# Performance work log

Measured on AMD Instinct MI355X. Metric: run time of the kernel, lower is better.

Reference implementation:

```python
import jax, jax.numpy as jnp
import numpy as np

B, L1, L2, H = 8, 384, 384, 128


def _lin(k, out_f, in_f, scale=0.05):
    kw, kb = jax.random.split(k)
    return (jax.random.normal(kw, (out_f, in_f), jnp.float32) * scale,
            jax.random.normal(kb, (out_f,), jnp.float32) * scale)


def setup_inputs() -> dict:
    key = jax.random.key(0)
    ks = jax.random.split(key, 10)
    Wq_w, Wq_b = _lin(ks[2], H, H)
    Wup_w, Wup_b = _lin(ks[3], H, H)
    Wvp_w, Wvp_b = _lin(ks[4], H, H)
    V_w, V_b = _lin(ks[5], 1, H)
    Wg_w, Wg_b = _lin(ks[6], 2 * H, 2 * H)
    W_ih, b_ih = _lin(ks[7], 4 * H, 2 * H)
    W_hh, b_hh = _lin(ks[8], 4 * H, H)
    return {
        "x": jax.random.normal(ks[0], (B, L1, H), jnp.float32),
        "x_mask": jnp.zeros((B, L1), dtype=bool),
        "y": jax.random.normal(ks[1], (B, L2, H), jnp.float32),
        "y_mask": jnp.zeros((B, L2), dtype=bool),
        "Wq_w": Wq_w, "Wq_b": Wq_b,
        "Wup_w": Wup_w, "Wup_b": Wup_b,
        "Wvp_w": Wvp_w, "Wvp_b": Wvp_b,
        "V_w": V_w, "V_b": V_b,
        "Wg_w": Wg_w, "Wg_b": Wg_b,
        "W_ih": W_ih, "W_hh": W_hh, "b_ih": b_ih, "b_hh": b_hh,
    }


def reference(x, x_mask, y, y_mask, Wq_w, Wq_b, Wup_w, Wup_b, Wvp_w, Wvp_b,
              V_w, V_b, Wg_w, Wg_b, W_ih, W_hh, b_ih, b_hh):
    b, l1, h = x.shape
    # projections (torch Linear: x @ W.T + b)
    x_proj = x @ Wup_w.T + Wup_b                      # [B, L1, H]
    y_proj = y @ Wq_w.T + Wq_b                        # [B, L2, H]
    # source feeds a constant zero hidden state into W_vp -> just its bias
    hidden_proj = jnp.zeros((h,), x.dtype) @ Wvp_w.T + Wvp_b  # [H]
    # additive attention scores: V . tanh(xp + yp + hp)
    sum_batch = jnp.tanh(x_proj[:, :, None, :] + y_proj[:, None, :, :] + hidden_proj)  # [B,L1,L2,H]
    s = jnp.einsum('btjh,h->btj', sum_batch, V_w[0]) + V_b[0]  # [B, L1, L2]
    # sum_mask = (1 - x_mask) outer (1 - y_mask)
    xm = 1.0 - x_mask.astype(s.dtype)
    ym = 1.0 - y_mask.astype(s.dtype)
    s = s * (xm[:, :, None] * ym[:, None, :])
    s = jnp.where(y_mask[:, None, :], -jnp.inf, s)
    alpha = jax.nn.softmax(s, axis=-1)                # [B, L1, L2]
    ct = jnp.einsum('btj,bjh->bth', alpha, y)         # [B, L1, H]
    merge = jnp.concatenate([x, ct], axis=2)          # [B, L1, 2H]
    gt = jax.nn.sigmoid(merge @ Wg_w.T + Wg_b)
    lstm_in = gt * merge                              # [B, L1, 2H]
    # single-layer unidirectional LSTM (torch gate order: i, f, g, o)
    gates_x = lstm_in @ W_ih.T + b_ih                 # [B, L1, 4H]

    def step(carry, gx):
        h_t, c_t = carry
        g = gx + h_t @ W_hh.T + b_hh
        i, f, gg, o = jnp.split(g, 4, axis=-1)
        c_n = jax.nn.sigmoid(f) * c_t + jax.nn.sigmoid(i) * jnp.tanh(gg)
        h_n = jax.nn.sigmoid(o) * jnp.tanh(c_n)
        return (h_n, c_n), h_n

    init = (jnp.zeros((b, h), x.dtype), jnp.zeros((b, h), x.dtype))
    _, hs = jax.lax.scan(step, init, jnp.swapaxes(gates_x, 0, 1))  # [L1, B, H]
    return jnp.swapaxes(hs, 0, 1)                     # [B, L1, H]
```

## Files before the change

### kernel.cpp

```cpp
#include <hip/hip_runtime.h>
#include <hip/hip_bf16.h>
#include <math.h>

typedef __attribute__((ext_vector_type(4))) float  float4v;
typedef __attribute__((ext_vector_type(2))) float  float2v;
typedef __attribute__((ext_vector_type(8))) short  short8;

#define B_ 8
#define L_ 384
#define H_ 128

__device__ __forceinline__ float bflo(unsigned int u){ unsigned int t = u << 16; float f; __builtin_memcpy(&f,&t,4); return f; }
__device__ __forceinline__ unsigned short f2bf(float f){
  unsigned int t; __builtin_memcpy(&t,&f,4);
  return (unsigned short)((t + 0x7fffu + ((t>>16)&1u)) >> 16);
}
__device__ __forceinline__ float fsig(float x){ return __fdividef(1.f, 1.f + __expf(-x)); }

__device__ __forceinline__ void barrier_lds(){
  asm volatile("s_waitcnt lgkmcnt(0)\n\ts_barrier" ::: "memory");
}

template<int K>
__device__ __forceinline__ void mfma_rowgemm_body(
    unsigned short* in_s,
    const float* __restrict__ inA,
    const float* __restrict__ W, const float* __restrict__ bias,
    const float* __restrict__ bias2, float* __restrict__ out,
    int Ntotal, int act, int row0, int ob)
{
  constexpr int KP = K + 2;
  const int tid  = threadIdx.x;
  const int w    = tid >> 6;
  const int l    = tid & 63;
  const int c    = l & 15;
  const int quad = l >> 4;

  #pragma unroll
  for (int it = 0; it < K/32; ++it) {
    int idx = it*256 + tid;
    int r = idx / (K/4);
    int k = (idx % (K/4)) * 4;
    float4v f = *(const float4v*)(inA + (size_t)(row0+r)*K + k);
    unsigned int p0 = (unsigned int)f2bf(f.x) | ((unsigned int)f2bf(f.y) << 16);
    unsigned int p1 = (unsigned int)f2bf(f.z) | ((unsigned int)f2bf(f.w) << 16);
    *(unsigned int*)&in_s[r*KP + k]     = p0;
    *(unsigned int*)&in_s[r*KP + k + 2] = p1;
  }

  const int n = ob + w*16 + c;
  short8 bfr[K/32];
  #pragma unroll
  for (int kt = 0; kt < K/32; ++kt) {
    const float* src = W + (size_t)n*K + kt*32 + quad*8;
    float4v f0 = *(const float4v*)(src);
    float4v f1 = *(const float4v*)(src + 4);
    short8 v;
    v[0]=(short)f2bf(f0[0]); v[1]=(short)f2bf(f0[1]); v[2]=(short)f2bf(f0[2]); v[3]=(short)f2bf(f0[3]);
    v[4]=(short)f2bf(f1[0]); v[5]=(short)f2bf(f1[1]); v[6]=(short)f2bf(f1[2]); v[7]=(short)f2bf(f1[3]);
    bfr[kt] = v;
  }
  __syncthreads();

  const float4v z4 = {0.f,0.f,0.f,0.f};
  float4v acc0 = z4, acc1 = z4;
  #pragma unroll
  for (int kt = 0; kt < K/32; ++kt) {
    short8 a0 = *(const short8*)&in_s[(c     )*KP + kt*32 + quad*8];
    short8 a1 = *(const short8*)&in_s[(16 + c)*KP + kt*32 + quad*8];
    acc0 = __builtin_amdgcn_mfma_f32_16x16x32_bf16(a0, bfr[kt], acc0, 0,0,0);
    acc1 = __builtin_amdgcn_mfma_f32_16x16x32_bf16(a1, bfr[kt], acc1, 0,0,0);
  }

  const float C2 = 2.8853900817779268f;
  float bv = bias[n] + (bias2 ? bias2[n] : 0.f);
  #pragma unroll
  for (int mt = 0; mt < 2; ++mt) {
    float4v A = mt ? acc1 : acc0;
    #pragma unroll
    for (int r = 0; r < 4; ++r) {
      int m = mt*16 + quad*4 + r;
      float val = A[r] + bv;
      if (act == 4)
        val = __builtin_amdgcn_exp2f(C2 * val);
      if (act == 3)
        out[(size_t)(row0+m)*Ntotal + (n & 127)*4 + (n >> 7)] = val;
      else
        out[(size_t)(row0+m)*Ntotal + n] = val;
    }
  }
}

template<int K>
__global__ __launch_bounds__(256) void mfma_rowgemm_kernel(
    const float* __restrict__ inA,
    const float* __restrict__ W, const float* __restrict__ bias,
    const float* __restrict__ bias2, float* __restrict__ out,
    int Ntotal, int act)
{
  __shared__ __align__(16) unsigned short in_s[32*(K+2)];
  mfma_rowgemm_body<K>(in_s, inA, W, bias, bias2, out,
                       Ntotal, act, blockIdx.x*32, blockIdx.y*64);
}

__global__ __launch_bounds__(256) void proj_mfma_kernel(
    const float* __restrict__ x, const float* __restrict__ y,
    const float* __restrict__ Wup_w, const float* __restrict__ Wup_b,
    const float* __restrict__ Wq_w, const float* __restrict__ Wq_b,
    const float* __restrict__ Wvp_b,
    float* __restrict__ xp, float* __restrict__ yp)
{
  __shared__ __align__(16) unsigned short in_s[32*130];
  int bx = blockIdx.x;
  if (bx < 192)
    mfma_rowgemm_body<128>(in_s, x, Wup_w, Wup_b, nullptr,
                           xp, 128, 4, (bx>>1)*32, (bx&1)*64);
  else {
    bx -= 192;
    mfma_rowgemm_body<128>(in_s, y, Wq_w, Wq_b, Wvp_b,
                           yp, 128, 4, (bx>>1)*32, (bx&1)*64);
  }
}

__global__ __launch_bounds__(256) void attn_kernel(
    const float* __restrict__ xp, const float* __restrict__ yp,
    const float* __restrict__ y, const unsigned char* __restrict__ xmask,
    const unsigned char* __restrict__ ymask, const float* __restrict__ Vw,
    const float* __restrict__ Vb,
    float* __restrict__ ctpbase, float* __restrict__ ml)
{
  __shared__ __align__(16) float xp_s[8][128];
  __shared__ __align__(16) float v2_s[128];
  __shared__ __align__(16) float yp_s[32][132];
  __shared__ __align__(16) float yc_s[32][132];
  __shared__ float xm_s[8];
  __shared__ float ym_s[32];
  __shared__ float sv_s;
  const int tid = threadIdx.x;
  const int b   = blockIdx.y;
  const int t0  = blockIdx.x * 8;
  const int jh  = blockIdx.z;
  const int jb  = jh * 96;
  {
    int r = tid >> 5, k4 = (tid & 31) * 4;
    float4v f = *(const float4v*)(xp + ((size_t)(b*L_ + t0 + r))*H_ + k4);
    *(float4v*)&xp_s[r][k4] = f;
    if (tid < 32) {
      float4v v = *(const float4v*)(Vw + tid*4);
      float4v v2; v2[0]=2.f*v[0]; v2[1]=2.f*v[1]; v2[2]=2.f*v[2]; v2[3]=2.f*v[3];
      *(float4v*)&v2_s[tid*4] = v2;
    }
    if (tid < 8) xm_s[tid] = xmask[b*L_ + t0 + tid] ? 0.f : 1.f;
  }
  __syncthreads();
  if (tid < 32) {
    float4v v = *(const float4v*)&v2_s[tid*4];
    float sm = (v[0]+v[1]) + (v[2]+v[3]);
    #pragma unroll
    for (int off = 16; off >= 1; off >>= 1) sm += __shfl_xor(sm, off);
    if (tid == 0) sv_s = 0.5f*sm + Vb[0];
  }

  float4v rp[4], ry[4];
  unsigned char ymb = 0;
  {
    #pragma unroll
    for (int it = 0; it < 4; ++it) {
      int idx = it*256 + tid; int r = idx >> 5; int k4 = (idx & 31) * 4;
      size_t base = ((size_t)(b*L_ + jb + r))*H_ + k4;
      rp[it] = *(const float4v*)(yp + base);
      ry[it] = *(const float4v*)(y + base);
    }
    if (tid < 32) ymb = ymask[b*L_ + jb + tid];
  }

  const int t = tid >> 5, u = tid & 31;
  float mrun = -__builtin_inff(), lrun = 0.f;
  float a0=0.f, a1=0.f, a2=0.f, a3=0.f;
  float svc = 0.f, xmv = 0.f;

  for (int c = 0; c < 3; ++c) {
    __syncthreads();
    #pragma unroll
    for (int it = 0; it < 4; ++it) {
      int idx = it*256 + tid; int r = idx >> 5; int k4 = (idx & 31) * 4;
      *(float4v*)&yp_s[r][k4] = rp[it];
      *(float4v*)&yc_s[r][k4] = ry[it];
    }
    if (tid < 32) ym_s[tid] = ymb ? 0.f : 1.f;
    __syncthreads();
    if (c == 0) { svc = sv_s; xmv = xm_s[t]; }
    if (c < 2) {
      #pragma unroll
      for (int it = 0; it < 4; ++it) {
        int idx = it*256 + tid; int r = idx >> 5; int k4 = (idx & 31) * 4;
        size_t base = ((size_t)(b*L_ + jb + (c+1)*32 + r))*H_ + k4;
        rp[it] = *(const float4v*)(yp + base);
        ry[it] = *(const float4v*)(y + base);
      }
      if (tid < 32) ymb = ymask[b*L_ + jb + (c+1)*32 + tid];
    }

    float sA = 0.f, sB = 0.f;
    {
      const float* yr = yp_s[u];
      const float* xr = xp_s[t];
      #pragma unroll 4
      for (int k = 0; k < 128; k += 4) {
        float4v yv = *(const float4v*)&yr[k];
        float4v xv = *(const float4v*)&xr[k];
        float4v vv = *(const float4v*)&v2_s[k];
        sA -= vv[0] * __builtin_amdgcn_rcpf(__builtin_fmaf(xv[0], yv[0], 1.f));
        sB -= vv[1] * __builtin_amdgcn_rcpf(__builtin_fmaf(xv[1], yv[1], 1.f));
        sA -= vv[2] * __builtin_amdgcn_rcpf(__builtin_fmaf(xv[2], yv[2], 1.f));
        sB -= vv[3] * __builtin_amdgcn_rcpf(__builtin_fmaf(xv[3], yv[3], 1.f));
      }
    }
    float ymv = ym_s[u];
    float s = (svc + sA + sB) * xmv * ymv;
    if (ymv == 0.f) s = -__builtin_inff();
    float mc = s;
    #pragma unroll
    for (int off = 16; off >= 1; off >>= 1) mc = fmaxf(mc, __shfl_xor(mc, off));
    float mnew = fmaxf(mrun, mc);
    float p  = __expf(s - mnew);
    float sc = __expf(mrun - mnew);
    float ps = p;
    #pragma unroll
    for (int off = 16; off >= 1; off >>= 1) ps += __shfl_xor(ps, off);
    lrun = lrun * sc + ps;
    mrun = mnew;
    a0 *= sc; a1 *= sc; a2 *= sc; a3 *= sc;
    #pragma unroll 8
    for (int j = 0; j < 32; ++j) {
      float pv = __shfl(p, j, 32);
      float4v yv = *(const float4v*)&yc_s[j][u*4];
      a0 += pv*yv[0]; a1 += pv*yv[1]; a2 += pv*yv[2]; a3 += pv*yv[3];
    }
  }
  const int row = b*L_ + t0 + t;
  float* ctp = ctpbase + (size_t)jh*393216;
  float4v ov; ov[0]=a0; ov[1]=a1; ov[2]=a2; ov[3]=a3;
  *(float4v*)(ctp + (size_t)row*H_ + u*4) = ov;
  if (u == 0) {
    ml[(jh*2+0)*3072 + row] = mrun;
    ml[(jh*2+1)*3072 + row] = lrun;
  }
}

__global__ __launch_bounds__(256) void gate1_kernel(
    const float* __restrict__ x,
    const float* __restrict__ ctpbase, const float* __restrict__ ml,
    const float* __restrict__ Wg_w, const float* __restrict__ Wg_b,
    float* __restrict__ out)
{
  constexpr int K = 256, KP = 258;
  __shared__ __align__(16) unsigned short in_s[32*KP];
  const int tid  = threadIdx.x;
  const int w    = tid >> 6;
  const int l    = tid & 63;
  const int c    = l & 15;
  const int quad = l >> 4;
  const int row0 = blockIdx.x * 32;
  const int ob   = blockIdx.y * 64;

  #pragma unroll
  for (int it = 0; it < 8; ++it) {
    int idx = it*256 + tid;
    int r = idx >> 6;
    int k = (idx & 63) * 4;
    int row = row0 + r;
    float4v f;
    if (k < 128) {
      f = *(const float4v*)(x + (size_t)row*128 + k);
    } else {
      float m0 = ml[       row], l0 = ml[  3072 + row];
      float m1 = ml[2*3072+row], l1 = ml[3*3072 + row];
      float m2 = ml[4*3072+row], l2 = ml[5*3072 + row];
      float m3 = ml[6*3072+row], l3 = ml[7*3072 + row];
      float mm = fmaxf(fmaxf(m0, m1), fmaxf(m2, m3));
      float e0 = __expf(m0-mm), e1 = __expf(m1-mm);
      float e2 = __expf(m2-mm), e3 = __expf(m3-mm);
      float inv = __fdividef(1.f, (l0*e0 + l1*e1) + (l2*e2 + l3*e3));
      size_t off = (size_t)row*128 + (k-128);
      float4v v0 = *(const float4v*)(ctpbase             + off);
      float4v v1 = *(const float4v*)(ctpbase +   393216  + off);
      float4v v2 = *(const float4v*)(ctpbase + 2*393216  + off);
      float4v v3 = *(const float4v*)(ctpbase + 3*393216  + off);
      f[0] = ((v0[0]*e0 + v1[0]*e1) + (v2[0]*e2 + v3[0]*e3))*inv;
      f[1] = ((v0[1]*e0 + v1[1]*e1) + (v2[1]*e2 + v3[1]*e3))*inv;
      f[2] = ((v0[2]*e0 + v1[2]*e1) + (v2[2]*e2 + v3[2]*e3))*inv;
      f[3] = ((v0[3]*e0 + v1[3]*e1) + (v2[3]*e2 + v3[3]*e3))*inv;
    }
    unsigned int p0 = (unsigned int)f2bf(f[0]) | ((unsigned int)f2bf(f[1]) << 16);
    unsigned int p1 = (unsigned int)f2bf(f[2]) | ((unsigned int)f2bf(f[3]) << 16);
    *(unsigned int*)&in_s[r*KP + k]     = p0;
    *(unsigned int*)&in_s[r*KP + k + 2] = p1;
  }

  const int n = ob + w*16 + c;
  short8 bfr[8];
  #pragma unroll
  for (int kt = 0; kt < 8; ++kt) {
    const float* src = Wg_w + (size_t)n*K + kt*32 + quad*8;
    float4v f0 = *(const float4v*)(src);
    float4v f1 = *(const float4v*)(src + 4);
    short8 v;
    v[0]=(short)f2bf(f0[0]); v[1]=(short)f2bf(f0[1]); v[2]=(short)f2bf(f0[2]); v[3]=(short)f2bf(f0[3]);
    v[4]=(short)f2bf(f1[0]); v[5]=(short)f2bf(f1[1]); v[6]=(short)f2bf(f1[2]); v[7]=(short)f2bf(f1[3]);
    bfr[kt] = v;
  }
  __syncthreads();

  const float4v z4 = {0.f,0.f,0.f,0.f};
  float4v acc0 = z4, acc1 = z4;
  #pragma unroll
  for (int kt = 0; kt < 8; ++kt) {
    short8 a0 = *(const short8*)&in_s[(c     )*KP + kt*32 + quad*8];
    short8 a1 = *(const short8*)&in_s[(16 + c)*KP + kt*32 + quad*8];
    acc0 = __builtin_amdgcn_mfma_f32_16x16x32_bf16(a0, bfr[kt], acc0, 0,0,0);
    acc1 = __builtin_amdgcn_mfma_f32_16x16x32_bf16(a1, bfr[kt], acc1, 0,0,0);
  }

  float bv = Wg_b[n];
  #pragma unroll
  for (int mt = 0; mt < 2; ++mt) {
    float4v A = mt ? acc1 : acc0;
    #pragma unroll
    for (int r = 0; r < 4; ++r) {
      int m = mt*16 + quad*4 + r;
      float val = A[r] + bv;
      float mg = bflo((unsigned int)in_s[m*KP + n]);
      out[(size_t)(row0+m)*256 + n] = fsig(val) * mg;
    }
  }
}

__global__ __launch_bounds__(512) void lstm_kernel(
    const float* __restrict__ gx, const float* __restrict__ Whh,
    float* __restrict__ out)
{
  __shared__ __align__(16) unsigned short h_s[2][128];
  const int tid  = threadIdx.x;
  const int b    = blockIdx.x;
  const int w    = tid >> 6;
  const int l    = tid & 63;
  const int col  = l & 15;
  const int quad = l >> 4;

  short8 bf[4][4];
  #pragma unroll
  for (int nt = 0; nt < 4; ++nt) {
    const int n = nt*128 + w*16 + col;
    #pragma unroll
    for (int kt = 0; kt < 4; ++kt) {
      const int k0 = kt*32 + quad*8;
      const float* src = Whh + (size_t)n*H_ + k0;
      float4v f0 = *(const float4v*)(src);
      float4v f1 = *(const float4v*)(src + 4);
      short8 v;
      v[0]=(short)f2bf(f0[0]); v[1]=(short)f2bf(f0[1]); v[2]=(short)f2bf(f0[2]); v[3]=(short)f2bf(f0[3]);
      v[4]=(short)f2bf(f1[0]); v[5]=(short)f2bf(f1[1]); v[6]=(short)f2bf(f1[2]); v[7]=(short)f2bf(f1[3]);
      bf[nt][kt] = v;
    }
  }

  if (tid < 128) { h_s[0][tid] = 0; h_s[1][tid] = 0; }
  float cst = 0.f;
  const int goff = w*16 + col;
  const float* gbase = gx + (size_t)b*L_*512 + goff*4;
  float* outp = out + (size_t)b*L_*H_ + goff;
  float4v gbuf[4];
  #pragma unroll
  for (int s = 0; s < 4; ++s)
    gbuf[s] = *(const float4v*)(gbase + (size_t)s*512);
  const float4v z4 = {0.f,0.f,0.f,0.f};
  const float NL2E = -1.4426950408889634f;
  const float P2L2E = 2.8853900817779268f;
  __syncthreads();

  for (int t4 = 0; t4 < L_; t4 += 4) {
    #pragma unroll
    for (int s = 0; s < 4; ++s) {
      const int tstep = t4 + s;
      const unsigned short* hb = h_s[s & 1];
      short8 a[4];
      #pragma unroll
      for (int kt=0;kt<4;++kt) a[kt] = *(const short8*)&hb[kt*32 + quad*8];
      float4v c0 = z4, c1 = z4, c2 = z4, c3 = z4;
      #pragma unroll
      for (int kt=0;kt<4;++kt) {
        c0 = __builtin_amdgcn_mfma_f32_16x16x32_bf16(a[kt], bf[0][kt], c0, 0,0,0);
        c1 = __builtin_amdgcn_mfma_f32_16x16x32_bf16(a[kt], bf[1][kt], c1, 0,0,0);
        c2 = __builtin_amdgcn_mfma_f32_16x16x32_bf16(a[kt], bf[2][kt], c2, 0,0,0);
        c3 = __builtin_amdgcn_mfma_f32_16x16x32_bf16(a[kt], bf[3][kt], c3, 0,0,0);
      }
      float g0 = c0[0] + gbuf[s][0];
      float g1 = c1[0] + gbuf[s][1];
      float g2 = c2[0] + gbuf[s][2];
      float g3 = c3[0] + gbuf[s][3];
      if (tstep + 4 < L_)
        gbuf[s] = *(const float4v*)(gbase + (size_t)(tstep+4)*512);
      if (quad == 0) {
        float ig = __builtin_amdgcn_rcpf(1.f + __builtin_amdgcn_exp2f(NL2E*g0));
        float fg = __builtin_amdgcn_rcpf(1.f + __builtin_amdgcn_exp2f(NL2E*g1));
        float gg = 1.f - 2.f*__builtin_amdgcn_rcpf(__builtin_amdgcn_exp2f(P2L2E*g2) + 1.f);
        float og = __builtin_amdgcn_rcpf(1.f + __builtin_amdgcn_exp2f(NL2E*g3));
        cst = fg*cst + ig*gg;
        float hn = og * (1.f - 2.f*__builtin_amdgcn_rcpf(__builtin_amdgcn_exp2f(P2L2E*cst) + 1.f));
        outp[(size_t)tstep*H_] = hn;
        h_s[(s+1)&1][goff] = f2bf(hn);
      }
      barrier_lds();
    }
  }
}

extern "C" void kernel_launch(void* const* d_in, const int* in_sizes, int n_in,
                              void* d_out, int out_size, void* d_ws, size_t ws_size,
                              hipStream_t stream)
{
  (void)in_sizes; (void)n_in; (void)out_size; (void)ws_size;
  const float* x     = (const float*)d_in[0];
  const unsigned char* xm = (const unsigned char*)d_in[1];
  const float* y     = (const float*)d_in[2];
  const unsigned char* ym = (const unsigned char*)d_in[3];
  const float* Wq_w  = (const float*)d_in[4];
  const float* Wq_b  = (const float*)d_in[5];
  const float* Wup_w = (const float*)d_in[6];
  const float* Wup_b = (const float*)d_in[7];
  const float* Wvp_b = (const float*)d_in[9];
  const float* V_w   = (const float*)d_in[10];
  const float* V_b   = (const float*)d_in[11];
  const float* Wg_w  = (const float*)d_in[12];
  const float* Wg_b  = (const float*)d_in[13];
  const float* W_ih  = (const float*)d_in[14];
  const float* W_hh  = (const float*)d_in[15];
  const float* b_ih  = (const float*)d_in[16];
  const float* b_hh  = (const float*)d_in[17];
  float* out = (float*)d_out;

  float* wsf    = (float*)d_ws;
  float* xp_ws  = wsf;
  float* yp_ws  = xp_ws + 393216;
  float* li_ws  = xp_ws;
  float* ctp_ws = yp_ws + 393216;
  float* gx_ws  = ctp_ws + 4*393216;
  float* ml_ws  = gx_ws + 1572864;

  proj_mfma_kernel<<<dim3(384),256,0,stream>>>(x, y, Wup_w, Wup_b, Wq_w, Wq_b, Wvp_b, xp_ws, yp_ws);
  attn_kernel<<<dim3(48,8,4),256,0,stream>>>(xp_ws, yp_ws, y, xm, ym, V_w, V_b, ctp_ws, ml_ws);
  gate1_kernel<<<dim3(96,4),256,0,stream>>>(x, ctp_ws, ml_ws, Wg_w, Wg_b, li_ws);
  mfma_rowgemm_kernel<256><<<dim3(96,8),256,0,stream>>>(li_ws, W_ih, b_ih, b_hh, gx_ws, 512, 3);
  lstm_kernel<<<dim3(8),512,0,stream>>>(gx_ws, W_hh, out);
}
```

Baseline: 336.6 us.

## Compute attention-weighted context with bf16 MFMA instead of scalar FMA loop

Replaces the per-thread scalar accumulation of alpha·y with 16x16x32 bf16 MFMA instructions. Probabilities are written to shared memory as bf16, padded to 16 rows, and y is loaded straight from global into register fragments converted to bf16, which removes the yc_s shared tile. This adds an extra barrier per chunk, uses half of the MFMA rows as padding, and lowers the precision of the context product to bf16.

```diff
diff --git a/kernel.cpp b/kernel.cpp
--- a/kernel.cpp
+++ b/kernel.cpp
@@ -132,7 +132,8 @@
   __shared__ __align__(16) float xp_s[8][128];
   __shared__ __align__(16) float v2_s[128];
   __shared__ __align__(16) float yp_s[32][132];
-  __shared__ __align__(16) float yc_s[32][132];
+  __shared__ __align__(16) unsigned short p_s[16][40];
+  __shared__ float sc_s[16];
   __shared__ float xm_s[8];
   __shared__ float ym_s[32];
   __shared__ float sv_s;
@@ -141,6 +142,10 @@
   const int t0  = blockIdx.x * 8;
   const int jh  = blockIdx.z;
   const int jb  = jh * 96;
+  const int w    = tid >> 6;
+  const int l    = tid & 63;
+  const int c16  = l & 15;
+  const int quad = l >> 4;
   {
     int r = tid >> 5, k4 = (tid & 31) * 4;
     float4v f = *(const float4v*)(xp + ((size_t)(b*L_ + t0 + r))*H_ + k4);
@@ -151,6 +156,8 @@
       *(float4v*)&v2_s[tid*4] = v2;
     }
     if (tid < 8) xm_s[tid] = xmask[b*L_ + t0 + tid] ? 0.f : 1.f;
+    if (tid < 16) sc_s[tid] = 0.f;
+    for (int i = 320 + tid; i < 640; i += 256) ((unsigned short*)p_s)[i] = 0;
   }
   __syncthreads();
   if (tid < 32) {
@@ -161,22 +168,21 @@
     if (tid == 0) sv_s = 0.5f*sm + Vb[0];
   }
 
-  float4v rp[4], ry[4];
+  float4v rp[4];
   unsigned char ymb = 0;
   {
     #pragma unroll
     for (int it = 0; it < 4; ++it) {
       int idx = it*256 + tid; int r = idx >> 5; int k4 = (idx & 31) * 4;
-      size_t base = ((size_t)(b*L_ + jb + r))*H_ + k4;
-      rp[it] = *(const float4v*)(yp + base);
-      ry[it] = *(const float4v*)(y + base);
+      rp[it] = *(const float4v*)(yp + ((size_t)(b*L_ + jb + r))*H_ + k4);
     }
     if (tid < 32) ymb = ymask[b*L_ + jb + tid];
   }
 
   const int t = tid >> 5, u = tid & 31;
   float mrun = -__builtin_inff(), lrun = 0.f;
-  float a0=0.f, a1=0.f, a2=0.f, a3=0.f;
+  const float4v z4 = {0.f,0.f,0.f,0.f};
+  float4v acc0 = z4, acc1 = z4;
   float svc = 0.f, xmv = 0.f;
 
   for (int c = 0; c < 3; ++c) {
@@ -185,18 +191,24 @@
     for (int it = 0; it < 4; ++it) {
       int idx = it*256 + tid; int r = idx >> 5; int k4 = (idx & 31) * 4;
       *(float4v*)&yp_s[r][k4] = rp[it];
-      *(float4v*)&yc_s[r][k4] = ry[it];
     }
     if (tid < 32) ym_s[tid] = ymb ? 0.f : 1.f;
     __syncthreads();
     if (c == 0) { svc = sv_s; xmv = xm_s[t]; }
+    short8 yb0, yb1;
+    {
+      const float* ybase = y + ((size_t)(b*L_ + jb + c*32 + quad*8))*H_ + c16;
+      #pragma unroll
+      for (int jj = 0; jj < 8; ++jj) {
+        yb0[jj] = (short)f2bf(ybase[(size_t)jj*H_ + w*16]);
+        yb1[jj] = (short)f2bf(ybase[(size_t)jj*H_ + (w+4)*16]);
+      }
+    }
     if (c < 2) {
       #pragma unroll
       for (int it = 0; it < 4; ++it) {
         int idx = it*256 + tid; int r = idx >> 5; int k4 = (idx & 31) * 4;
-        size_t base = ((size_t)(b*L_ + jb + (c+1)*32 + r))*H_ + k4;
-        rp[it] = *(const float4v*)(yp + base);
-        ry[it] = *(const float4v*)(y + base);
+        rp[it] = *(const float4v*)(yp + ((size_t)(b*L_ + jb + (c+1)*32 + r))*H_ + k4);
       }
       if (tid < 32) ymb = ymask[b*L_ + jb + (c+1)*32 + tid];
     }
@@ -230,19 +242,28 @@
     for (int off = 16; off >= 1; off >>= 1) ps += __shfl_xor(ps, off);
     lrun = lrun * sc + ps;
     mrun = mnew;
-    a0 *= sc; a1 *= sc; a2 *= sc; a3 *= sc;
-    #pragma unroll 8
-    for (int j = 0; j < 32; ++j) {
-      float pv = __shfl(p, j, 32);
-      float4v yv = *(const float4v*)&yc_s[j][u*4];
-      a0 += pv*yv[0]; a1 += pv*yv[1]; a2 += pv*yv[2]; a3 += pv*yv[3];
-    }
-  }
-  const int row = b*L_ + t0 + t;
+    p_s[t][u] = f2bf(p);
+    if (u == 0) sc_s[t] = sc;
+    __syncthreads();
+    short8 pf = *(const short8*)&p_s[c16][quad*8];
+    float4v scv;
+    #pragma unroll
+    for (int r = 0; r < 4; ++r) scv[r] = sc_s[quad*4 + r];
+    acc0 *= scv; acc1 *= scv;
+    acc0 = __builtin_amdgcn_mfma_f32_16x16x32_bf16(pf, yb0, acc0, 0,0,0);
+    acc1 = __builtin_amdgcn_mfma_f32_16x16x32_bf16(pf, yb1, acc1, 0,0,0);
+  }
   float* ctp = ctpbase + (size_t)jh*393216;
-  float4v ov; ov[0]=a0; ov[1]=a1; ov[2]=a2; ov[3]=a3;
-  *(float4v*)(ctp + (size_t)row*H_ + u*4) = ov;
+  if (quad < 2) {
+    #pragma unroll
+    for (int r = 0; r < 4; ++r) {
+      int row = b*L_ + t0 + quad*4 + r;
+      ctp[(size_t)row*H_ + w*16 + c16]     = acc0[r];
+      ctp[(size_t)row*H_ + (w+4)*16 + c16] = acc1[r];
+    }
+  }
   if (u == 0) {
+    int row = b*L_ + t0 + t;
     ml[(jh*2+0)*3072 + row] = mrun;
     ml[(jh*2+1)*3072 + row] = lrun;
   }
```

Result: no change. 331.5 us (-1.5%).
